# Performance work log

Measured on AMD Instinct MI355X. Metric: run time of the kernel, lower is better.

The kernel has to match this reference:

```python
import jax, jax.numpy as jnp
import numpy as np

N_SAMPLES = 256   # n_samples from __init__
N_THIN = 10       # N from __init__
N_WORDS = 4096


def setup_inputs() -> dict:
    key = jax.random.key(0)
    k1, k2, k3 = jax.random.split(key, 3)
    # scale potentials so per-step weight deltas stay in a sane exp() range
    bigram = jax.random.normal(k1, (N_WORDS, N_WORDS), dtype=jnp.float32)
    start = jax.random.normal(k2, (N_WORDS,), dtype=jnp.float32)
    end = jax.random.normal(k3, (N_WORDS,), dtype=jnp.float32)
    return {"n_words": N_WORDS, "bigram": bigram, "start": start, "end": end}


def _mh_chain(bigram, start, end, n_words, chain_size, rng):
    # chain[0] = identity permutation (random_start=False)
    perm0 = jnp.arange(n_words, dtype=jnp.int32)
    w0 = bigram[perm0[:-1], perm0[1:]].sum() + start[perm0[0]] + end[perm0[-1]]

    def step(carry, k):
        perm, w_last = carry
        k_pos, k_cat, k_u = jax.random.split(k, 3)
        # pick a token to move, remove it -> perm2 of length n_words-1
        pos = jax.random.randint(k_pos, (), 0, n_words)
        to_move = perm[pos]
        j = jnp.arange(n_words - 1)
        perm2 = perm[j + (j >= pos).astype(j.dtype)]
        # insertion logits over n_words slots (self._probs, unnormalized log p)
        logits = jnp.zeros((n_words,), dtype=bigram.dtype)
        logits = logits.at[0].add(start[to_move]).at[-1].add(end[to_move])
        logits = logits.at[1:].add(bigram[perm2, to_move])   # left-neighbor term
        logits = logits.at[:-1].add(bigram[to_move, perm2])  # right-neighbor term
        p = jax.nn.softmax(logits)
        new_pos = jax.random.categorical(k_cat, logits)
        # insert to_move at new_pos
        jj = jnp.arange(n_words)
        shifted = perm2[jnp.clip(jj - (jj > new_pos).astype(jj.dtype), 0, n_words - 2)]
        sample = jnp.where(jj == new_pos, to_move, shifted).astype(perm.dtype)
        # new chain weight
        new_w = bigram[sample[:-1], sample[1:]].sum() + start[sample[0]] + end[sample[-1]]
        # MH accept ratio; removing to_move from sample recovers perm2, so the
        # reverse insertion distribution equals p -> ratio p[new_pos]/p[pos]
        acc = jnp.minimum(1.0, jnp.exp(new_w - w_last) * p[new_pos] / p[pos])
        accept = acc > jax.random.uniform(k_u, ())
        perm_next = jnp.where(accept, sample, perm)
        w_next = jnp.where(accept, new_w, w_last)
        return (perm_next, w_next), perm_next

    keys = jax.random.split(rng, chain_size - 1)
    _, perms = jax.lax.scan(step, (perm0, w0), keys)
    chain = jnp.concatenate([perm0[None, :], perms], axis=0)  # [chain_size, n_words]
    sel = jnp.arange(0, chain_size, N_THIN) + (N_THIN - 1)    # thin: every N-th state
    return chain[sel]


def reference(n_words, bigram, start, end):
    chain_size = N_SAMPLES * N_THIN
    rng = jax.random.key(42)
    return _mh_chain(bigram, start, end, n_words, chain_size, rng)
```

## Files before the change

kernel.cpp:

```cpp
#include <hip/hip_runtime.h>
#include <stdint.h>


#define NW 4096
#define NSTEPS 2559
#define NTHREADS 1024
#define NWAVES 16

typedef unsigned long long u64;
typedef uint32_t u32;
typedef unsigned short u16;

__device__ __forceinline__ u32 rotl32(u32 v, u32 r) { return (v << r) | (v >> (32u - r)); }

__device__ __forceinline__ void tf2x32(u32 k0, u32 k1, u32 x0, u32 x1, u32* o0, u32* o1) {
  u32 ks2 = k0 ^ k1 ^ 0x1BD11BDAu;
  x0 += k0; x1 += k1;
#define TFR(r0, r1, r2, r3)                      \
  x0 += x1; x1 = rotl32(x1, r0); x1 ^= x0;       \
  x0 += x1; x1 = rotl32(x1, r1); x1 ^= x0;       \
  x0 += x1; x1 = rotl32(x1, r2); x1 ^= x0;       \
  x0 += x1; x1 = rotl32(x1, r3); x1 ^= x0;
  TFR(13, 15, 26, 6)  x0 += k1;  x1 += ks2 + 1u;
  TFR(17, 29, 16, 24) x0 += ks2; x1 += k0 + 2u;
  TFR(13, 15, 26, 6)  x0 += k0;  x1 += k1 + 3u;
  TFR(17, 29, 16, 24) x0 += k1;  x1 += ks2 + 4u;
  TFR(13, 15, 26, 6)  x0 += ks2; x1 += k0 + 5u;
#undef TFR
  *o0 = x0; *o1 = x1;
}

__device__ __forceinline__ float unif01(u32 bits) {
  return __uint_as_float((bits >> 9) | 0x3f800000u) - 1.0f;
}

__device__ __forceinline__ u32 fkey(float f) {
  u32 b = __float_as_uint(f);
  return b ^ ((b >> 31) ? 0xFFFFFFFFu : 0x80000000u);
}


template <int CTRL>
__device__ __forceinline__ u32 dpp32(u32 v) {
  return (u32)__builtin_amdgcn_update_dpp(0, (int)v, CTRL, 0xF, 0xF, true);
}

template <int CTRL>
__device__ __forceinline__ void dppmax64(u32& hi, u32& lo) {
  u32 h2 = dpp32<CTRL>(hi);
  u32 l2 = dpp32<CTRL>(lo);
  bool g = (h2 > hi) || (h2 == hi && l2 > lo);
  hi = g ? h2 : hi;
  lo = g ? l2 : lo;
}

__device__ __forceinline__ u64 wave_max_u64(u64 key) {
  u32 lo = (u32)key, hi = (u32)(key >> 32);
  dppmax64<0x111>(hi, lo); dppmax64<0x112>(hi, lo);
  dppmax64<0x114>(hi, lo); dppmax64<0x118>(hi, lo);
  dppmax64<0x142>(hi, lo); dppmax64<0x143>(hi, lo);
  return ((u64)hi << 32) | lo;
}

__device__ __forceinline__ u64 bfly16_max_u64(u64 key) {
  u32 lo = (u32)key, hi = (u32)(key >> 32);
  dppmax64<0xB1>(hi, lo); dppmax64<0x4E>(hi, lo);
  dppmax64<0x141>(hi, lo); dppmax64<0x140>(hi, lo);
  return ((u64)hi << 32) | lo;
}


#define TT 32
__global__ void transpose_k(const float* __restrict__ in, float* __restrict__ out) {
  __shared__ float tile[TT][TT + 1];
  int x = blockIdx.x * TT + threadIdx.x;
  int y = blockIdx.y * TT + threadIdx.y;
  for (int j = 0; j < TT; j += 8) tile[threadIdx.y + j][threadIdx.x] = in[(u64)(y + j) * NW + x];
  __syncthreads();
  x = blockIdx.y * TT + threadIdx.x;
  y = blockIdx.x * TT + threadIdx.y;
  for (int j = 0; j < TT; j += 8) out[(u64)(y + j) * NW + x] = tile[threadIdx.x][threadIdx.y + j];
}

__global__ void gumbel_k(float* __restrict__ gumb) {
  long long idx = (long long)blockIdx.x * blockDim.x + threadIdx.x;
  if (idx >= (long long)NSTEPS * NW) return;
  int t = (int)(idx >> 12);
  int i = (int)(idx & (NW - 1));
  u32 kt0, kt1, kc0, kc1, ba, bb;
  tf2x32(0u, 42u, 0u, (u32)t, &kt0, &kt1);
  tf2x32(kt0, kt1, 0u, 1u, &kc0, &kc1);
  tf2x32(kc0, kc1, 0u, (u32)i, &ba, &bb);
  float u = unif01(ba ^ bb);
  if (u == 0.0f) u = 1.17549435e-38f;
  float t1 = (float)log((double)u);
  float t2 = (float)log((double)(-t1));
  gumb[idx] = -t2;
}

__global__ void posu_k(int* __restrict__ posArr, float* __restrict__ uArr) {
  int t = blockIdx.x * blockDim.x + threadIdx.x;
  if (t >= NSTEPS) return;
  u32 kt0, kt1, kp0, kp1, ku0, ku1, k2a, k2b, ra, rb, ua, ub;
  tf2x32(0u, 42u, 0u, (u32)t, &kt0, &kt1);
  tf2x32(kt0, kt1, 0u, 0u, &kp0, &kp1);
  tf2x32(kt0, kt1, 0u, 2u, &ku0, &ku1);
  tf2x32(kp0, kp1, 0u, 1u, &k2a, &k2b);
  tf2x32(k2a, k2b, 0u, 0u, &ra, &rb);
  posArr[t] = (int)((ra ^ rb) & (u32)(NW - 1));
  tf2x32(ku0, ku1, 0u, 0u, &ua, &ub);
  uArr[t] = unif01(ua ^ ub);
}


#define SAMPLE_AT(idx)                                                        \
  ((idx) < np ? (int)s_perm[(idx) + ((idx) >= pos)]                           \
              : ((idx) == np ? tm                                             \
                             : (int)s_perm[((idx)-1) + (((idx)-1) >= pos)]))

__global__ __launch_bounds__(NTHREADS)
void mcmc_fast12(const float* __restrict__ bigram,
                 const float* __restrict__ bigT,
                 const float* __restrict__ gumb,
                 const int* __restrict__ posArr,
                 const float* __restrict__ uArr,
                 const float* __restrict__ startv,
                 const float* __restrict__ endv,
                 int* __restrict__ out) {
  __shared__ u16    s_perm[NW];
  __shared__ float2 s_rows[NW];
  __shared__ float  s_pairw[NW];
  __shared__ u64    s_redu[NWAVES];
  __shared__ float  s_stm, s_etm, s_lpos, s_brgS, s_vn1, s_vn2;
  __shared__ int    s_accs;

  const int tid = threadIdx.x;
  const int lane = tid & 63;
  const int wid = tid >> 6;
  const int j0 = tid * 4;

  for (int i = tid; i < NW; i += NTHREADS) s_perm[i] = (u16)i;
#pragma unroll
  for (int k = 0; k < 4; ++k) {
    int j = j0 + k;
    s_pairw[j] = (j < NW - 1) ? bigram[(u64)j * NW + (j + 1)] : 0.0f;
  }

  int pos = posArr[0];
  int tm = pos;
  {
    float4 rb4 = ((const float4*)(bigram + (u64)tm * NW))[tid];
    float4 rt4 = ((const float4*)(bigT + (u64)tm * NW))[tid];
    ((float4*)(&s_rows[j0]))[0] = make_float4(rt4.x, rb4.x, rt4.y, rb4.y);
    ((float4*)(&s_rows[j0]))[1] = make_float4(rt4.z, rb4.z, rt4.w, rb4.w);
  }
  if (tid == 0) { s_stm = startv[tm]; s_etm = endv[tm]; }

  float u_cur = uArr[0];
  float start_cur = startv[0];
  float end_cur = endv[NW - 1];

  float4 g4 = ((const float4*)gumb)[tid];
  __syncthreads();

  for (int t = 0; t < NSTEPS; ++t) {
    const float gg[4] = {g4.x, g4.y, g4.z, g4.w};
    int pos_nxt; float u_nxt;
    {
      int tn = (t + 1 < NSTEPS) ? (t + 1) : (NSTEPS - 1);
      g4 = ((const float4*)(gumb + ((u64)tn << 12)))[tid];
      pos_nxt = posArr[tn];
      u_nxt = uArr[tn];
    }
    const int tmR = (int)s_perm[pos_nxt];
    const float4 rbR = ((const float4*)(bigram + (u64)tmR * NW))[tid];
    const float4 rtR = ((const float4*)(bigT + (u64)tmR * NW))[tid];
    float stmR = 0.0f, etmR = 0.0f;
    if (tid == 0) { stmR = startv[tmR]; etmR = endv[tmR]; }

    ushort4 pq = ((const ushort4*)s_perm)[tid];
    const int p0i = pq.x, p1i = pq.y, p2i = pq.z, p3i = pq.w;
    int pm1, pp4;
    {
      u32 lo = (u32)pq.x | ((u32)pq.y << 16);
      u32 hi = (u32)pq.z | ((u32)pq.w << 16);
      pm1 = (int)(dpp32<0x138>(hi) >> 16);
      pp4 = (int)(dpp32<0x130>(lo) & 0xFFFFu);
      if (lane == 0)  pm1 = (tid > 0) ? (int)s_perm[j0 - 1] : 0;
      if (lane == 63) pp4 = (tid < NTHREADS - 1) ? (int)s_perm[j0 + 4] : 0;
    }
    float4 pwq = ((const float4*)s_pairw)[tid];
    float pwm1, pwp4;
    {
      pwm1 = __uint_as_float(dpp32<0x138>(__float_as_uint(pwq.w)));
      pwp4 = __uint_as_float(dpp32<0x130>(__float_as_uint(pwq.x)));
      if (lane == 0)  pwm1 = (tid > 0) ? s_pairw[j0 - 1] : 0.0f;
      if (lane == 63) pwp4 = (tid < NTHREADS - 1) ? s_pairw[j0 + 4] : 0.0f;
    }

    float stm_r = 0.0f, etm_r = 0.0f, remL = 0.0f, remR = 0.0f, brgv = 0.0f;
    float sv0m = 0.0f, ev1m = 0.0f;
    if (wid == 0) {
      stm_r = s_stm; etm_r = s_etm;
      int pl = (pos > 0) ? (int)s_perm[pos - 1] : 0;
      int pr = (pos < NW - 1) ? (int)s_perm[pos + 1] : 0;
      if (pos > 0)      remL = s_rows[pl].x;
      if (pos < NW - 1) remR = s_rows[pr].y;
      if (pos > 0 && pos < NW - 1) brgv = bigram[(u64)pl * NW + pr];
      sv0m = startv[(int)s_perm[(0 >= pos) ? 1 : 0]];
      ev1m = endv[(int)s_perm[(NW - 2) + ((NW - 2) >= pos)]];
      if (lane == 0) s_brgS = brgv;
    }

    const int w0 = (j0     >= pos) ? p1i : p0i;
    const int w1 = (j0 + 1 >= pos) ? p2i : p1i;
    const int w2 = (j0 + 2 >= pos) ? p3i : p2i;
    const int w3 = (j0 + 3 >= pos) ? pp4 : p3i;
    const int wprev = ((j0 - 1) >= pos) ? p0i : pm1;
    const float2 f0 = s_rows[w0];
    const float2 f1 = s_rows[w1];
    const float2 f2 = s_rows[w2];
    const float2 f3 = s_rows[w3];
    float tprev = __uint_as_float(dpp32<0x138>(__float_as_uint(f3.x)));
    if (lane == 0 && tid > 0) tprev = s_rows[wprev].x;
    float li0 = tprev + f0.y;
    float li1 = f0.x + f1.y;
    float li2 = f1.x + f2.y;
    float li3 = f2.x + f3.y;
    if (tid == 0)            li0 = s_stm + f0.y;
    if (tid == NTHREADS - 1) li3 = s_etm + f2.x;
    if ((pos >> 2) == tid) {
      int k = pos & 3;
      s_lpos = (k == 0) ? li0 : ((k == 1) ? li1 : ((k == 2) ? li2 : li3));
    }
    u64 best;
    {
      u64 b0 = ((u64)fkey(gg[0] + li0) << 32) | (u32)(NW - 1 - j0);
      u64 b1 = ((u64)fkey(gg[1] + li1) << 32) | (u32)(NW - 2 - j0);
      u64 b2 = ((u64)fkey(gg[2] + li2) << 32) | (u32)(NW - 3 - j0);
      u64 b3 = ((u64)fkey(gg[3] + li3) << 32) | (u32)(NW - 4 - j0);
      best = b0 > b1 ? b0 : b1;
      u64 b23 = b2 > b3 ? b2 : b3;
      if (b23 > best) best = b23;
    }
    best = wave_max_u64(best);
    if (lane == 63) s_redu[wid] = best;
    __syncthreads();

    int np;
    {
      u64 bb = bfly16_max_u64(s_redu[lane & 15]);
      np = NW - 1 - (int)(bb & 0xFFFFFFFFu);
    }
    const int tmA = SAMPLE_AT(pos_nxt);
    ushort4 st;
    st.x = (j0     < np) ? (u16)w0 : ((j0     == np) ? (u16)tm : (u16)wprev);
    st.y = (j0 + 1 < np) ? (u16)w1 : ((j0 + 1 == np) ? (u16)tm : (u16)w0);
    st.z = (j0 + 2 < np) ? (u16)w2 : ((j0 + 2 == np) ? (u16)tm : (u16)w1);
    st.w = (j0 + 3 < np) ? (u16)w3 : ((j0 + 3 == np) ? (u16)tm : (u16)w2);
    const float brgAll = s_brgS;
    float nv0, nv1, nv2, nv3;
    {
      float vA0 = (j0     < pos - 1) ? pwq.x : pwq.y;
      float vB0 = (j0 - 1 < pos - 1) ? pwm1  : pwq.x;
      nv0 = (j0 < np) ? vA0 : vB0;
      int kk0 = (j0 < np) ? j0 : j0 - 1;
      if (kk0 == pos - 1) nv0 = brgAll;

      float vA1 = (j0 + 1 < pos - 1) ? pwq.y : pwq.z;
      float vB1 = (j0     < pos - 1) ? pwq.x : pwq.y;
      nv1 = (j0 + 1 < np) ? vA1 : vB1;
      int kk1 = (j0 + 1 < np) ? j0 + 1 : j0;
      if (kk1 == pos - 1) nv1 = brgAll;

      float vA2 = (j0 + 2 < pos - 1) ? pwq.z : pwq.w;
      float vB2 = (j0 + 1 < pos - 1) ? pwq.y : pwq.z;
      nv2 = (j0 + 2 < np) ? vA2 : vB2;
      int kk2 = (j0 + 2 < np) ? j0 + 2 : j0 + 1;
      if (kk2 == pos - 1) nv2 = brgAll;

      float vA3 = (j0 + 3 < pos - 1) ? pwq.w : pwp4;
      float vB3 = (j0 + 2 < pos - 1) ? pwq.z : pwq.w;
      nv3 = (j0 + 3 < np) ? vA3 : vB3;
      int kk3 = (j0 + 3 < np) ? j0 + 3 : j0 + 2;
      if (kk3 == pos - 1) nv3 = brgAll;
    }
    if (wid == 0) {
      int ls_i = (np >= 1) ? ((np - 1) + ((np - 1) >= pos)) : 0;
      int rs_i = (np <= NW - 2) ? (np + (np >= pos)) : 0;
      const int l_s = (int)s_perm[ls_i];
      const int r_s = (int)s_perm[rs_i];
      float vnpm1 = (np >= 1)      ? s_rows[l_s].x : 0.0f;
      float vnp   = (np <= NW - 2) ? s_rows[r_s].y : 0.0f;
      float splitv = 0.0f;
      if (np > 0 && np < NW - 1) {
        int k_s = (np - 1) + ((np - 1) >= pos);
        splitv = (np == pos) ? brgv : s_pairw[k_s];
      }
      float sv0 = (np > 0) ? sv0m : stm_r;
      float ev1 = (np < NW - 1) ? ev1m : etm_r;
      float lposv = s_lpos;
      double delta = 0.0;
      if (pos > 0)                 delta -= (double)remL;
      if (pos < NW - 1)            delta -= (double)remR;
      if (pos > 0 && pos < NW - 1) delta += (double)brgv;
      if (np > 0)                  delta += (double)vnpm1;
      if (np < NW - 1)             delta += (double)vnp;
      if (np > 0 && np < NW - 1)   delta -= (double)splitv;
      delta += ((double)sv0 - (double)start_cur) + ((double)ev1 - (double)end_cur);
      float lnp = (np == 0) ? (stm_r + vnp)
                : ((np == NW - 1) ? (etm_r + vnpm1) : (vnpm1 + vnp));
      double ed = delta + ((double)lnp - (double)lposv);
      float a = fminf(1.0f, expf((float)ed));
      int acc = (a > u_cur) ? 1 : 0;
      if (lane == 0) { s_accs = acc; s_vn1 = vnpm1; s_vn2 = vnp; }
      if (acc) { start_cur = sv0; end_cur = ev1; }
    }
    __syncthreads();

    const int acc = s_accs;
    const int tm_next = acc ? tmA : tmR;
    float4 rb = rbR, rt = rtR;
    if (acc) {
      rb = ((const float4*)(bigram + (u64)tm_next * NW))[tid];
      rt = ((const float4*)(bigT + (u64)tm_next * NW))[tid];
    }
    if (tid == 0) {
      s_stm = acc ? startv[tm_next] : stmR;
      s_etm = acc ? endv[tm_next] : etmR;
    }
    if (acc) {
      ((ushort4*)s_perm)[tid] = st;
      float vn1 = s_vn1, vn2 = s_vn2;
      float o0 = (j0     == np - 1) ? vn1 : ((j0     == np) ? vn2 : nv0);
      float o1 = (j0 + 1 == np - 1) ? vn1 : ((j0 + 1 == np) ? vn2 : nv1);
      float o2 = (j0 + 2 == np - 1) ? vn1 : ((j0 + 2 == np) ? vn2 : nv2);
      float o3 = (j0 + 3 == np - 1) ? vn1 : ((j0 + 3 == np) ? vn2 : nv3);
      if (j0 + 3 >= NW - 1) o3 = 0.0f;
      ((float4*)s_pairw)[tid] = make_float4(o0, o1, o2, o3);
    }
    ((float4*)(&s_rows[j0]))[0] = make_float4(rt.x, rb.x, rt.y, rb.y);
    ((float4*)(&s_rows[j0]))[1] = make_float4(rt.z, rb.z, rt.w, rb.w);
    tm = tm_next;
    pos = pos_nxt;
    u_cur = u_nxt;
    __syncthreads();

    if ((t % 10) == 8) {
      int row = (t - 8) / 10;
      ushort4 p4 = ((const ushort4*)s_perm)[tid];
      int4 o4;
      o4.x = (int)p4.x; o4.y = (int)p4.y; o4.z = (int)p4.z; o4.w = (int)p4.w;
      ((int4*)(out + (u64)row * NW))[tid] = o4;
    }
  }
}


__global__ __launch_bounds__(NTHREADS)
void mcmc_kernel(const float* __restrict__ bigram,
                 const float* __restrict__ startv,
                 const float* __restrict__ endv,
                 int* __restrict__ out) {
  __shared__ int    s_perm[NW];
  __shared__ float  s_logit[NW];
  __shared__ float  s_gath[NW];
  __shared__ float  s_redf[NWAVES];
  __shared__ u64    s_redu[NWAVES];
  __shared__ double s_redd[NWAVES];
  __shared__ float  s_m, s_Z, s_w;
  __shared__ int    s_pos, s_tm, s_np, s_acc;
  __shared__ u32    s_kcat0, s_kcat1, s_ku0, s_ku1;

  const int tid = threadIdx.x;
  const int lane = tid & 63;
  const int wid = tid >> 6;

  for (int i = tid; i < NW; i += NTHREADS) s_perm[i] = i;
  for (int j = tid; j < NW - 1; j += NTHREADS) s_gath[j] = bigram[(u64)j * NW + (j + 1)];
  __syncthreads();
  if (tid == 0) {
    float S = 0.0f;
    for (int j = 0; j < NW - 1; ++j) S += s_gath[j];
    S = S + startv[0];
    S = S + endv[NW - 1];
    s_w = S;
  }
  __syncthreads();

  for (int t = 0; t < NSTEPS; ++t) {
    if (tid == 0) {
      u32 kt0, kt1;
      tf2x32(0u, 42u, 0u, (u32)t, &kt0, &kt1);
      u32 kp0, kp1, kc0, kc1, ku0, ku1;
      tf2x32(kt0, kt1, 0u, 0u, &kp0, &kp1);
      tf2x32(kt0, kt1, 0u, 1u, &kc0, &kc1);
      tf2x32(kt0, kt1, 0u, 2u, &ku0, &ku1);
      u32 k2a, k2b, ra, rb;
      tf2x32(kp0, kp1, 0u, 1u, &k2a, &k2b);
      tf2x32(k2a, k2b, 0u, 0u, &ra, &rb);
      int pos = (int)((ra ^ rb) & (u32)(NW - 1));
      s_pos = pos;
      s_tm = s_perm[pos];
      s_kcat0 = kc0; s_kcat1 = kc1; s_ku0 = ku0; s_ku1 = ku1;
    }
    __syncthreads();
    const int pos = s_pos, tm = s_tm;

    float lmax = -3.402823466e+38f;
    for (int i = tid; i < NW; i += NTHREADS) {
      float li;
      if (i == 0) {
        int r = s_perm[(0 >= pos) ? 1 : 0];
        li = startv[tm] + bigram[(u64)tm * NW + r];
      } else if (i == NW - 1) {
        int l = s_perm[((NW - 2) >= pos) ? (NW - 1) : (NW - 2)];
        li = endv[tm] + bigram[(u64)l * NW + tm];
      } else {
        int l = s_perm[((i - 1) >= pos) ? i : (i - 1)];
        int r = s_perm[(i >= pos) ? (i + 1) : i];
        li = bigram[(u64)l * NW + tm] + bigram[(u64)tm * NW + r];
      }
      s_logit[i] = li;
      lmax = fmaxf(lmax, li);
    }
    for (int o = 32; o > 0; o >>= 1) lmax = fmaxf(lmax, __shfl_down(lmax, o, 64));
    if (lane == 0) s_redf[wid] = lmax;
    __syncthreads();
    if (tid == 0) {
      float m = s_redf[0];
      for (int w = 1; w < NWAVES; ++w) m = fmaxf(m, s_redf[w]);
      s_m = m;
    }
    __syncthreads();
    const float m = s_m;

    double zacc = 0.0;
    u64 best = 0;
    const u32 kc0 = s_kcat0, kc1 = s_kcat1;
    for (int i = tid; i < NW; i += NTHREADS) {
      float li = s_logit[i];
      float ex = (float)exp((double)(li - m));
      zacc += (double)ex;
      u32 ba, bb;
      tf2x32(kc0, kc1, 0u, (u32)i, &ba, &bb);
      float u = unif01(ba ^ bb);
      if (u == 0.0f) u = 1.17549435e-38f;
      float t1 = (float)log((double)u);
      float t2 = (float)log((double)(-t1));
      float g = -t2;
      float sv = g + li;
      u64 key = ((u64)fkey(sv) << 32) | (u32)(NW - 1 - i);
      if (key > best) best = key;
    }
    for (int o = 32; o > 0; o >>= 1) {
      u64 w = __shfl_down(best, o, 64);
      if (w > best) best = w;
      zacc += __shfl_down(zacc, o, 64);
    }
    if (lane == 0) { s_redu[wid] = best; s_redd[wid] = zacc; }
    __syncthreads();
    if (tid == 0) {
      u64 b = s_redu[0]; double z = s_redd[0];
      for (int w = 1; w < NWAVES; ++w) {
        if (s_redu[w] > b) b = s_redu[w];
        z += s_redd[w];
      }
      s_np = NW - 1 - (int)(b & 0xFFFFFFFFu);
      s_Z = (float)z;
    }
    __syncthreads();
    const int np = s_np;

    for (int j = tid; j < NW - 1; j += NTHREADS) {
      int a = (j < np) ? s_perm[j + (j >= pos)]
                       : ((j == np) ? tm : s_perm[(j - 1) + ((j - 1) >= pos)]);
      int j1 = j + 1;
      int b = (j1 < np) ? s_perm[j1 + (j1 >= pos)]
                        : ((j1 == np) ? tm : s_perm[(j1 - 1) + ((j1 - 1) >= pos)]);
      s_gath[j] = bigram[(u64)a * NW + b];
    }
    __syncthreads();

    if (tid == 0) {
      float S = 0.0f;
      for (int j = 0; j < NW - 1; ++j) S += s_gath[j];
      int s0 = (0 < np) ? s_perm[(0 >= pos) ? 1 : 0] : tm;
      int sl = ((NW - 1) == np) ? tm : s_perm[(NW - 2) + ((NW - 2) >= pos)];
      S = S + startv[s0];
      S = S + endv[sl];
      float dw = S - s_w;
      float e1 = (float)exp((double)dw);
      float en = (float)exp((double)(s_logit[np] - m));
      float eo = (float)exp((double)(s_logit[pos] - m));
      float pn = en / s_Z;
      float po = eo / s_Z;
      float acc = e1 * pn;
      acc = acc / po;
      acc = fminf(1.0f, acc);
      u32 ua, ub;
      tf2x32(s_ku0, s_ku1, 0u, 0u, &ua, &ub);
      float u = unif01(ua ^ ub);
      int accept = (acc > u) ? 1 : 0;
      s_acc = accept;
      if (accept) s_w = S;
    }
    __syncthreads();

    int stash[4];
    if (s_acc) {
      for (int k = 0; k < 4; ++k) {
        int i = tid + k * NTHREADS;
        stash[k] = (i < np) ? s_perm[i + (i >= pos)]
                            : ((i == np) ? tm : s_perm[(i - 1) + ((i - 1) >= pos)]);
      }
    }
    __syncthreads();
    if (s_acc) {
      for (int k = 0; k < 4; ++k) {
        int i = tid + k * NTHREADS;
        s_perm[i] = stash[k];
      }
    }
    __syncthreads();

    if (((t + 1) % 10) == 9) {
      int row = (t - 8) / 10;
      for (int i = tid; i < NW; i += NTHREADS) out[(u64)row * NW + i] = s_perm[i];
    }
    __syncthreads();
  }
}

extern "C" void kernel_launch(void* const* d_in, const int* in_sizes, int n_in,
                              void* d_out, int out_size, void* d_ws, size_t ws_size,
                              hipStream_t stream) {
  const float* bigram = (const float*)d_in[1];
  const float* startv = (const float*)d_in[2];
  const float* endv   = (const float*)d_in[3];
  int* out = (int*)d_out;

  const size_t needT = (size_t)NW * NW * sizeof(float);
  const size_t needG = (size_t)NSTEPS * NW * sizeof(float);
  const size_t needP = (size_t)NSTEPS * (sizeof(int) + sizeof(float));

  if (ws_size >= needT + needG + needP) {
    float* bigT = (float*)d_ws;
    float* gumb = (float*)((char*)d_ws + needT);
    int* posArr = (int*)((char*)d_ws + needT + needG);
    float* uArr = (float*)((char*)d_ws + needT + needG + (size_t)NSTEPS * sizeof(int));
    hipLaunchKernelGGL(transpose_k, dim3(NW / TT, NW / TT), dim3(TT, 8), 0, stream,
                       bigram, bigT);
    long long ng = (long long)NSTEPS * NW;
    hipLaunchKernelGGL(gumbel_k, dim3((unsigned)((ng + 255) / 256)), dim3(256), 0, stream,
                       gumb);
    hipLaunchKernelGGL(posu_k, dim3((NSTEPS + 255) / 256), dim3(256), 0, stream,
                       posArr, uArr);
    hipLaunchKernelGGL(mcmc_fast12, dim3(1), dim3(NTHREADS), 0, stream,
                       bigram, bigT, gumb, posArr, uArr, startv, endv, out);
  } else {
    hipLaunchKernelGGL(mcmc_kernel, dim3(1), dim3(NTHREADS), 0, stream,
                       bigram, startv, endv, out);
  }
}
```

Measured before the change: 7.056 ms.

## Keep perm/pairw slices in registers and defer accept-only work into branch

The per-thread slices of the permutation and pair weights now stay in registers across steps instead of being re-read from shared memory each iteration. The position and uniform values are prefetched two steps ahead. Computation of the new permutation slice and pair weights moves inside the accept branch, so rejected steps skip it. Only wave 0 does the post-reduction scalar work and broadcasts tmA through shared memory. This shortens the serial per-step critical path of the single-block chain, at the cost of more register pressure and a redundant reduction recompute on accept.

```diff
diff --git a/kernel.cpp b/kernel.cpp
--- a/kernel.cpp
+++ b/kernel.cpp
@@ -119,7 +119,7 @@
                              : (int)s_perm[((idx)-1) + (((idx)-1) >= pos)]))
 
 __global__ __launch_bounds__(NTHREADS)
-void mcmc_fast12(const float* __restrict__ bigram,
+void mcmc_fast13(const float* __restrict__ bigram,
                  const float* __restrict__ bigT,
                  const float* __restrict__ gumb,
                  const int* __restrict__ posArr,
@@ -132,7 +132,7 @@
   __shared__ float  s_pairw[NW];
   __shared__ u64    s_redu[NWAVES];
   __shared__ float  s_stm, s_etm, s_lpos, s_brgS, s_vn1, s_vn2;
-  __shared__ int    s_accs;
+  __shared__ int    s_accs, s_tmA;
 
   const int tid = threadIdx.x;
   const int lane = tid & 63;
@@ -140,13 +140,18 @@
   const int j0 = tid * 4;
 
   for (int i = tid; i < NW; i += NTHREADS) s_perm[i] = (u16)i;
-#pragma unroll
-  for (int k = 0; k < 4; ++k) {
-    int j = j0 + k;
-    s_pairw[j] = (j < NW - 1) ? bigram[(u64)j * NW + (j + 1)] : 0.0f;
-  }
+  ushort4 pq = make_ushort4((u16)j0, (u16)(j0 + 1), (u16)(j0 + 2), (u16)(j0 + 3));
+  float4 pwq;
+  pwq.x = bigram[(u64)j0 * NW + (j0 + 1)];
+  pwq.y = bigram[(u64)(j0 + 1) * NW + (j0 + 2)];
+  pwq.z = bigram[(u64)(j0 + 2) * NW + (j0 + 3)];
+  pwq.w = (j0 + 3 < NW - 1) ? bigram[(u64)(j0 + 3) * NW + (j0 + 4)] : 0.0f;
+  ((float4*)s_pairw)[tid] = pwq;
 
   int pos = posArr[0];
+  int pn1 = posArr[1];
+  float u_cur = uArr[0];
+  float un1 = uArr[1];
   int tm = pos;
   {
     float4 rb4 = ((const float4*)(bigram + (u64)tm * NW))[tid];
@@ -156,7 +161,6 @@
   }
   if (tid == 0) { s_stm = startv[tm]; s_etm = endv[tm]; }
 
-  float u_cur = uArr[0];
   float start_cur = startv[0];
   float end_cur = endv[NW - 1];
 
@@ -165,39 +169,19 @@
 
   for (int t = 0; t < NSTEPS; ++t) {
     const float gg[4] = {g4.x, g4.y, g4.z, g4.w};
-    int pos_nxt; float u_nxt;
-    {
-      int tn = (t + 1 < NSTEPS) ? (t + 1) : (NSTEPS - 1);
-      g4 = ((const float4*)(gumb + ((u64)tn << 12)))[tid];
-      pos_nxt = posArr[tn];
-      u_nxt = uArr[tn];
-    }
-    const int tmR = (int)s_perm[pos_nxt];
+    const int tmR = (int)s_perm[pn1];
     const float4 rbR = ((const float4*)(bigram + (u64)tmR * NW))[tid];
     const float4 rtR = ((const float4*)(bigT + (u64)tmR * NW))[tid];
     float stmR = 0.0f, etmR = 0.0f;
     if (tid == 0) { stmR = startv[tmR]; etmR = endv[tmR]; }
-
-    ushort4 pq = ((const ushort4*)s_perm)[tid];
-    const int p0i = pq.x, p1i = pq.y, p2i = pq.z, p3i = pq.w;
-    int pm1, pp4;
+    int pn2; float un2;
     {
-      u32 lo = (u32)pq.x | ((u32)pq.y << 16);
-      u32 hi = (u32)pq.z | ((u32)pq.w << 16);
-      pm1 = (int)(dpp32<0x138>(hi) >> 16);
-      pp4 = (int)(dpp32<0x130>(lo) & 0xFFFFu);
-      if (lane == 0)  pm1 = (tid > 0) ? (int)s_perm[j0 - 1] : 0;
-      if (lane == 63) pp4 = (tid < NTHREADS - 1) ? (int)s_perm[j0 + 4] : 0;
-    }
-    float4 pwq = ((const float4*)s_pairw)[tid];
-    float pwm1, pwp4;
-    {
-      pwm1 = __uint_as_float(dpp32<0x138>(__float_as_uint(pwq.w)));
-      pwp4 = __uint_as_float(dpp32<0x130>(__float_as_uint(pwq.x)));
-      if (lane == 0)  pwm1 = (tid > 0) ? s_pairw[j0 - 1] : 0.0f;
-      if (lane == 63) pwp4 = (tid < NTHREADS - 1) ? s_pairw[j0 + 4] : 0.0f;
-    }
-
+      int tn = (t + 1 < NSTEPS) ? (t + 1) : (NSTEPS - 1);
+      int tn2 = (t + 2 < NSTEPS) ? (t + 2) : (NSTEPS - 1);
+      g4 = ((const float4*)(gumb + ((u64)tn << 12)))[tid];
+      pn2 = posArr[tn2];
+      un2 = uArr[tn2];
+    }
     float stm_r = 0.0f, etm_r = 0.0f, remL = 0.0f, remR = 0.0f, brgv = 0.0f;
     float sv0m = 0.0f, ev1m = 0.0f;
     if (wid == 0) {
@@ -211,6 +195,20 @@
       ev1m = endv[(int)s_perm[(NW - 2) + ((NW - 2) >= pos)]];
       if (lane == 0) s_brgS = brgv;
     }
+
+    const int p0i = pq.x, p1i = pq.y, p2i = pq.z, p3i = pq.w;
+    int pm1, pp4;
+    {
+      u32 lo = (u32)pq.x | ((u32)pq.y << 16);
+      u32 hi = (u32)pq.z | ((u32)pq.w << 16);
+      pm1 = (int)(dpp32<0x138>(hi) >> 16);
+      pp4 = (int)(dpp32<0x130>(lo) & 0xFFFFu);
+      if (lane == 0)  pm1 = (tid > 0) ? (int)s_perm[j0 - 1] : 0;
+      if (lane == 63) pp4 = (tid < NTHREADS - 1) ? (int)s_perm[j0 + 4] : 0;
+    }
+    float pwm1_e = 0.0f, pwp4_e = 0.0f;
+    if (lane == 0 && tid > 0) pwm1_e = s_pairw[j0 - 1];
+    if (lane == 63 && tid < NTHREADS - 1) pwp4_e = s_pairw[j0 + 4];
 
     const int w0 = (j0     >= pos) ? p1i : p0i;
     const int w1 = (j0 + 1 >= pos) ? p2i : p1i;
@@ -247,56 +245,21 @@
     if (lane == 63) s_redu[wid] = best;
     __syncthreads();
 
-    int np;
-    {
+    if (wid == 0) {
       u64 bb = bfly16_max_u64(s_redu[lane & 15]);
-      np = NW - 1 - (int)(bb & 0xFFFFFFFFu);
-    }
-    const int tmA = SAMPLE_AT(pos_nxt);
-    ushort4 st;
-    st.x = (j0     < np) ? (u16)w0 : ((j0     == np) ? (u16)tm : (u16)wprev);
-    st.y = (j0 + 1 < np) ? (u16)w1 : ((j0 + 1 == np) ? (u16)tm : (u16)w0);
-    st.z = (j0 + 2 < np) ? (u16)w2 : ((j0 + 2 == np) ? (u16)tm : (u16)w1);
-    st.w = (j0 + 3 < np) ? (u16)w3 : ((j0 + 3 == np) ? (u16)tm : (u16)w2);
-    const float brgAll = s_brgS;
-    float nv0, nv1, nv2, nv3;
-    {
-      float vA0 = (j0     < pos - 1) ? pwq.x : pwq.y;
-      float vB0 = (j0 - 1 < pos - 1) ? pwm1  : pwq.x;
-      nv0 = (j0 < np) ? vA0 : vB0;
-      int kk0 = (j0 < np) ? j0 : j0 - 1;
-      if (kk0 == pos - 1) nv0 = brgAll;
-
-      float vA1 = (j0 + 1 < pos - 1) ? pwq.y : pwq.z;
-      float vB1 = (j0     < pos - 1) ? pwq.x : pwq.y;
-      nv1 = (j0 + 1 < np) ? vA1 : vB1;
-      int kk1 = (j0 + 1 < np) ? j0 + 1 : j0;
-      if (kk1 == pos - 1) nv1 = brgAll;
-
-      float vA2 = (j0 + 2 < pos - 1) ? pwq.z : pwq.w;
-      float vB2 = (j0 + 1 < pos - 1) ? pwq.y : pwq.z;
-      nv2 = (j0 + 2 < np) ? vA2 : vB2;
-      int kk2 = (j0 + 2 < np) ? j0 + 2 : j0 + 1;
-      if (kk2 == pos - 1) nv2 = brgAll;
-
-      float vA3 = (j0 + 3 < pos - 1) ? pwq.w : pwp4;
-      float vB3 = (j0 + 2 < pos - 1) ? pwq.z : pwq.w;
-      nv3 = (j0 + 3 < np) ? vA3 : vB3;
-      int kk3 = (j0 + 3 < np) ? j0 + 3 : j0 + 2;
-      if (kk3 == pos - 1) nv3 = brgAll;
-    }
-    if (wid == 0) {
+      const int np = NW - 1 - (int)(bb & 0xFFFFFFFFu);
       int ls_i = (np >= 1) ? ((np - 1) + ((np - 1) >= pos)) : 0;
       int rs_i = (np <= NW - 2) ? (np + (np >= pos)) : 0;
       const int l_s = (int)s_perm[ls_i];
       const int r_s = (int)s_perm[rs_i];
-      float vnpm1 = (np >= 1)      ? s_rows[l_s].x : 0.0f;
-      float vnp   = (np <= NW - 2) ? s_rows[r_s].y : 0.0f;
+      const int tmA = SAMPLE_AT(pn1);
       float splitv = 0.0f;
       if (np > 0 && np < NW - 1) {
         int k_s = (np - 1) + ((np - 1) >= pos);
         splitv = (np == pos) ? brgv : s_pairw[k_s];
       }
+      float vnpm1 = (np >= 1)      ? s_rows[l_s].x : 0.0f;
+      float vnp   = (np <= NW - 2) ? s_rows[r_s].y : 0.0f;
       float sv0 = (np > 0) ? sv0m : stm_r;
       float ev1 = (np < NW - 1) ? ev1m : etm_r;
       float lposv = s_lpos;
@@ -313,46 +276,83 @@
       double ed = delta + ((double)lnp - (double)lposv);
       float a = fminf(1.0f, expf((float)ed));
       int acc = (a > u_cur) ? 1 : 0;
-      if (lane == 0) { s_accs = acc; s_vn1 = vnpm1; s_vn2 = vnp; }
+      if (lane == 0) { s_accs = acc; s_vn1 = vnpm1; s_vn2 = vnp; s_tmA = tmA; }
       if (acc) { start_cur = sv0; end_cur = ev1; }
     }
     __syncthreads();
 
     const int acc = s_accs;
-    const int tm_next = acc ? tmA : tmR;
+    int tm_next = tmR;
     float4 rb = rbR, rt = rtR;
+    ushort4 st = pq;
     if (acc) {
+      tm_next = s_tmA;
       rb = ((const float4*)(bigram + (u64)tm_next * NW))[tid];
       rt = ((const float4*)(bigT + (u64)tm_next * NW))[tid];
-    }
-    if (tid == 0) {
-      s_stm = acc ? startv[tm_next] : stmR;
-      s_etm = acc ? endv[tm_next] : etmR;
-    }
-    if (acc) {
+      u64 bb = bfly16_max_u64(s_redu[lane & 15]);
+      const int np = NW - 1 - (int)(bb & 0xFFFFFFFFu);
+      st.x = (j0     < np) ? (u16)w0 : ((j0     == np) ? (u16)tm : (u16)wprev);
+      st.y = (j0 + 1 < np) ? (u16)w1 : ((j0 + 1 == np) ? (u16)tm : (u16)w0);
+      st.z = (j0 + 2 < np) ? (u16)w2 : ((j0 + 2 == np) ? (u16)tm : (u16)w1);
+      st.w = (j0 + 3 < np) ? (u16)w3 : ((j0 + 3 == np) ? (u16)tm : (u16)w2);
       ((ushort4*)s_perm)[tid] = st;
-      float vn1 = s_vn1, vn2 = s_vn2;
+      float pwm1 = __uint_as_float(dpp32<0x138>(__float_as_uint(pwq.w)));
+      float pwp4 = __uint_as_float(dpp32<0x130>(__float_as_uint(pwq.x)));
+      if (lane == 0)  pwm1 = pwm1_e;
+      if (lane == 63) pwp4 = pwp4_e;
+      const float brgAll = s_brgS;
+      float nv0, nv1, nv2, nv3;
+      {
+        float vA0 = (j0     < pos - 1) ? pwq.x : pwq.y;
+        float vB0 = (j0 - 1 < pos - 1) ? pwm1  : pwq.x;
+        nv0 = (j0 < np) ? vA0 : vB0;
+        int kk0 = (j0 < np) ? j0 : j0 - 1;
+        if (kk0 == pos - 1) nv0 = brgAll;
+
+        float vA1 = (j0 + 1 < pos - 1) ? pwq.y : pwq.z;
+        float vB1 = (j0     < pos - 1) ? pwq.x : pwq.y;
+        nv1 = (j0 + 1 < np) ? vA1 : vB1;
+        int kk1 = (j0 + 1 < np) ? j0 + 1 : j0;
+        if (kk1 == pos - 1) nv1 = brgAll;
+
+        float vA2 = (j0 + 2 < pos - 1) ? pwq.z : pwq.w;
+        float vB2 = (j0 + 1 < pos - 1) ? pwq.y : pwq.z;
+        nv2 = (j0 + 2 < np) ? vA2 : vB2;
+        int kk2 = (j0 + 2 < np) ? j0 + 2 : j0 + 1;
+        if (kk2 == pos - 1) nv2 = brgAll;
+
+        float vA3 = (j0 + 3 < pos - 1) ? pwq.w : pwp4;
+        float vB3 = (j0 + 2 < pos - 1) ? pwq.z : pwq.w;
+        nv3 = (j0 + 3 < np) ? vA3 : vB3;
+        int kk3 = (j0 + 3 < np) ? j0 + 3 : j0 + 2;
+        if (kk3 == pos - 1) nv3 = brgAll;
+      }
+      const float vn1 = s_vn1, vn2 = s_vn2;
       float o0 = (j0     == np - 1) ? vn1 : ((j0     == np) ? vn2 : nv0);
       float o1 = (j0 + 1 == np - 1) ? vn1 : ((j0 + 1 == np) ? vn2 : nv1);
       float o2 = (j0 + 2 == np - 1) ? vn1 : ((j0 + 2 == np) ? vn2 : nv2);
       float o3 = (j0 + 3 == np - 1) ? vn1 : ((j0 + 3 == np) ? vn2 : nv3);
       if (j0 + 3 >= NW - 1) o3 = 0.0f;
-      ((float4*)s_pairw)[tid] = make_float4(o0, o1, o2, o3);
+      pwq = make_float4(o0, o1, o2, o3);
+      ((float4*)s_pairw)[tid] = pwq;
+      if (tid == 0) { s_stm = startv[tm_next]; s_etm = endv[tm_next]; }
+    } else {
+      if (tid == 0) { s_stm = stmR; s_etm = etmR; }
     }
     ((float4*)(&s_rows[j0]))[0] = make_float4(rt.x, rb.x, rt.y, rb.y);
     ((float4*)(&s_rows[j0]))[1] = make_float4(rt.z, rb.z, rt.w, rb.w);
+    pq = st;
     tm = tm_next;
-    pos = pos_nxt;
-    u_cur = u_nxt;
-    __syncthreads();
+    pos = pn1; u_cur = un1;
+    pn1 = pn2; un1 = un2;
 
     if ((t % 10) == 8) {
       int row = (t - 8) / 10;
-      ushort4 p4 = ((const ushort4*)s_perm)[tid];
       int4 o4;
-      o4.x = (int)p4.x; o4.y = (int)p4.y; o4.z = (int)p4.z; o4.w = (int)p4.w;
+      o4.x = (int)pq.x; o4.y = (int)pq.y; o4.z = (int)pq.z; o4.w = (int)pq.w;
       ((int4*)(out + (u64)row * NW))[tid] = o4;
     }
+    __syncthreads();
   }
 }
 
@@ -556,7 +556,7 @@
                        gumb);
     hipLaunchKernelGGL(posu_k, dim3((NSTEPS + 255) / 256), dim3(256), 0, stream,
                        posArr, uArr);
-    hipLaunchKernelGGL(mcmc_fast12, dim3(1), dim3(NTHREADS), 0, stream,
+    hipLaunchKernelGGL(mcmc_fast13, dim3(1), dim3(NTHREADS), 0, stream,
                        bigram, bigT, gumb, posArr, uArr, startv, endv, out);
   } else {
     hipLaunchKernelGGL(mcmc_kernel, dim3(1), dim3(NTHREADS), 0, stream,
```

Measured after the change: 6.604 ms. 6.4% less time.
